# Optimization experiments

Hardware: AMD Instinct MI355X
Metric: run time of the kernel (lower is better)

Reference implementation:

```python
import jax, jax.numpy as jnp
import numpy as np


def setup_inputs() -> dict:
    key = jax.random.key(0)
    ks = jax.random.split(key, 12)
    B, T, E, H, D, NB, BS = 64, 1, 1280, 20, 64, 7, 64
    w = lambda k: jax.random.normal(k, (E, E), jnp.float32) * 0.02
    return {
        "hidden_states": jax.random.normal(ks[0], (B, T, E), jnp.float32),
        "kcache": jax.random.normal(ks[1], (B, H, NB, BS, D), jnp.float32),
        "vcache": jax.random.normal(ks[2], (B, H, NB, BS, D), jnp.float32),
        "wq": w(ks[3]), "bq": jax.random.normal(ks[4], (E,), jnp.float32) * 0.02,
        "wk": w(ks[5]), "bk": jnp.zeros((E,), jnp.float32),
        "wv": w(ks[6]), "bv": jax.random.normal(ks[7], (E,), jnp.float32) * 0.02,
        "wo": w(ks[8]), "bo": jax.random.normal(ks[9], (E,), jnp.float32) * 0.02,
        "cache_position": jax.random.randint(ks[10], (B,), 0, 447, jnp.int32),
        "block_tables": jax.random.randint(ks[11], (B, NB), 0, NB, jnp.int32),
    }


def reference(hidden_states, kcache, vcache, wq, bq, wk, bk, wv, bv, wo, bo,
              cache_position, block_tables):
    B, T, E = hidden_states.shape          # T == 1 (decode)
    _, H, NB, BS, D = kcache.shape
    L = NB * BS                             # max logical cache length (448)
    scaling = D ** -0.5

    # projections -> (B, H, T, D)
    q = (hidden_states @ wq.T + bq).reshape(B, T, H, D).transpose(0, 2, 1, 3) * scaling
    kn = (hidden_states @ wk.T + bk).reshape(B, T, H, D).transpose(0, 2, 1, 3)
    vn = (hidden_states @ wv.T + bv).reshape(B, T, H, D).transpose(0, 2, 1, 3)

    # paged block-table gather: logical cache (B, H, L, D)
    bt = block_tables[:, None, :, None, None].astype(jnp.int32)
    kc = jnp.take_along_axis(kcache, bt, axis=2).reshape(B, H, L, D)
    vc = jnp.take_along_axis(vcache, bt, axis=2).reshape(B, H, L, D)

    # insert the new token's k/v at position cache_position[b]
    pos = jnp.arange(L, dtype=jnp.int32)
    seq = cache_position.reshape(B, 1, 1, 1)
    at_new = pos.reshape(1, 1, L, 1) == seq          # (B,1,L,1)
    k_full = jnp.where(at_new, kn, kc)               # kn (B,H,1,D) broadcasts
    v_full = jnp.where(at_new, vn, vc)

    # causal decode: attend to positions <= cache_position
    scores = jnp.einsum('bhtd,bhld->bhtl', q, k_full)
    valid = pos.reshape(1, 1, 1, L) <= cache_position.reshape(B, 1, 1, 1)
    scores = jnp.where(valid, scores, jnp.finfo(scores.dtype).min)
    probs = jax.nn.softmax(scores, axis=-1)
    out = jnp.einsum('bhtl,bhld->bhtd', probs, v_full)

    out = out.transpose(0, 2, 1, 3).reshape(B, T, E)
    return out @ wo.T + bo
```

## Files before the change

kernel.cpp:

```cpp
#include <hip/hip_runtime.h>
#include <math.h>

#define E 1280
#define NHEAD 20
#define HD 64
#define NBLK 7
#define NBATCH 64

typedef __bf16 bf16x8 __attribute__((ext_vector_type(8)));
typedef float floatx4 __attribute__((ext_vector_type(4)));

__device__ __forceinline__ float wave_max64(float v) {
#pragma unroll
    for (int o = 32; o > 0; o >>= 1) v = fmaxf(v, __shfl_xor(v, o, 64));
    return v;
}
__device__ __forceinline__ float wave_sum64(float v) {
#pragma unroll
    for (int o = 32; o > 0; o >>= 1) v += __shfl_xor(v, o, 64);
    return v;
}
__device__ __forceinline__ bf16x8 cvt8(float4 lo, float4 hi) {
    bf16x8 r;
    r[0] = (__bf16)lo.x; r[1] = (__bf16)lo.y; r[2] = (__bf16)lo.z; r[3] = (__bf16)lo.w;
    r[4] = (__bf16)hi.x; r[5] = (__bf16)hi.y; r[6] = (__bf16)hi.z; r[7] = (__bf16)hi.w;
    return r;
}

template<int NTOT, bool QKV>
__global__ __launch_bounds__(256) void mfma_gemm(
    const float* __restrict__ A,
    const float* __restrict__ W0, const float* __restrict__ W1,
    const float* __restrict__ W2,
    const float* __restrict__ b0, const float* __restrict__ b1,
    const float* __restrict__ b2,
    float* __restrict__ C)
{
    __shared__ __align__(16) float Cred[4][64][16];

    const int t = threadIdx.x;
    const int lane = t & 63;
    const int wv = t >> 6;
    const int quad = lane >> 4;
    const int l16 = lane & 15;
    const int jg0 = blockIdx.x * 16;

    int j0; const float* Wp; const float* bp; float scl;
    if (QKV) {
        const int msel = jg0 / E;
        j0 = jg0 - msel * E;
        Wp = (msel == 0) ? W0 : ((msel == 1) ? W1 : W2);
        bp = (msel == 0) ? b0 : ((msel == 1) ? b1 : b2);
        scl = (msel == 0) ? 0.125f : 1.0f;
    } else { j0 = jg0; Wp = W0; bp = b0; scl = 1.0f; }

    const int kbeg = wv * (E / 4);
    const int ko = quad * 8;

    const float* __restrict__ wrow = Wp + (size_t)(j0 + l16) * E;
    const float* __restrict__ arow = A + (size_t)l16 * E;

    floatx4 acc[4] = {};
    float4 Ac[16], Wc[4];

    {
        const int k0 = kbeg;
#pragma unroll
        for (int rg = 0; rg < 4; ++rg) {
            const float* ar = arow + (size_t)rg * 16 * E + k0 + ko;
            Ac[rg * 4 + 0] = *(const float4*)(ar);
            Ac[rg * 4 + 1] = *(const float4*)(ar + 4);
            Ac[rg * 4 + 2] = *(const float4*)(ar + 32);
            Ac[rg * 4 + 3] = *(const float4*)(ar + 36);
        }
        const float* wr = wrow + k0 + ko;
        Wc[0] = *(const float4*)(wr);
        Wc[1] = *(const float4*)(wr + 4);
        Wc[2] = *(const float4*)(wr + 32);
        Wc[3] = *(const float4*)(wr + 36);
    }

#pragma unroll
    for (int c = 0; c < 5; ++c) {
        float4 An[16], Wn[4];
        if (c < 4) {
            const int k1 = kbeg + (c + 1) * 64;
#pragma unroll
            for (int rg = 0; rg < 4; ++rg) {
                const float* ar = arow + (size_t)rg * 16 * E + k1 + ko;
                An[rg * 4 + 0] = *(const float4*)(ar);
                An[rg * 4 + 1] = *(const float4*)(ar + 4);
                An[rg * 4 + 2] = *(const float4*)(ar + 32);
                An[rg * 4 + 3] = *(const float4*)(ar + 36);
            }
            const float* wr = wrow + k1 + ko;
            Wn[0] = *(const float4*)(wr);
            Wn[1] = *(const float4*)(wr + 4);
            Wn[2] = *(const float4*)(wr + 32);
            Wn[3] = *(const float4*)(wr + 36);
        }
        const bf16x8 bf0 = cvt8(Wc[0], Wc[1]);
        const bf16x8 bf1 = cvt8(Wc[2], Wc[3]);
#pragma unroll
        for (int rg = 0; rg < 4; ++rg) {
            acc[rg] = __builtin_amdgcn_mfma_f32_16x16x32_bf16(
                cvt8(Ac[rg * 4 + 0], Ac[rg * 4 + 1]), bf0, acc[rg], 0, 0, 0);
            acc[rg] = __builtin_amdgcn_mfma_f32_16x16x32_bf16(
                cvt8(Ac[rg * 4 + 2], Ac[rg * 4 + 3]), bf1, acc[rg], 0, 0, 0);
        }
        if (c < 4) {
#pragma unroll
            for (int i = 0; i < 16; ++i) Ac[i] = An[i];
#pragma unroll
            for (int i = 0; i < 4; ++i) Wc[i] = Wn[i];
        }
    }

#pragma unroll
    for (int rg = 0; rg < 4; ++rg)
#pragma unroll
        for (int r = 0; r < 4; ++r)
            Cred[wv][rg * 16 + quad * 4 + r][l16] = acc[rg][r];
    __syncthreads();
#pragma unroll
    for (int i = 0; i < 4; ++i) {
        const int e = t + i * 256;
        const int row = e >> 4, col = e & 15;
        float s = Cred[0][row][col] + Cred[1][row][col]
                + Cred[2][row][col] + Cred[3][row][col];
        C[(size_t)row * NTOT + jg0 + col] = (s + bp[j0 + col]) * scl;
    }
}

__global__ __launch_bounds__(256) void attn_kernel(
    const float* __restrict__ qkv,
    const float* __restrict__ kcache, const float* __restrict__ vcache,
    const int* __restrict__ cache_position, const int* __restrict__ block_tables,
    float* __restrict__ obuf)
{
    const int bh = blockIdx.x;
    const int b = bh / NHEAD;
    const int h = bh - b * NHEAD;
    const int lane = threadIdx.x & 63;
    const int wv = threadIdx.x >> 6;
    const int d4 = lane & 15;
    const int sg = lane >> 4;

    __shared__ __align__(16) float q_lds[64];
    __shared__ __align__(16) float o_lds[4][64];
    __shared__ float ml_lds[4][2];

    const int pos = cache_position[b];
    const int last = pos - 1;
    const int col = h * HD + lane;

    const float qd  = qkv[(size_t)b * (3 * E) + col];
    const float knd = qkv[(size_t)b * (3 * E) + E + col];
    const float vnd = qkv[(size_t)b * (3 * E) + 2 * E + col];
    if (wv == 0) q_lds[lane] = qd;
    __syncthreads();

    float m = -INFINITY, lsum = 0.0f;
    float4 vacc = make_float4(0.f, 0.f, 0.f, 0.f);

    const int nb0 = wv;
    const int nb1 = wv + 4;
    const bool hasb0 = (nb0 * 64 <= last);
    const bool hasb1 = (nb1 * 64 <= last);

    if (hasb0) {
        const size_t bhoff = (size_t)(b * NHEAD + h) * NBLK;
        const int phys0 = block_tables[b * NBLK + nb0];
        const float* __restrict__ Kb0 = kcache + ((bhoff + phys0) << 12);
        const float* __restrict__ Vb0 = vcache + ((bhoff + phys0) << 12);
        const float* __restrict__ Kb1 = Kb0;
        const float* __restrict__ Vb1 = Vb0;
        if (hasb1) {
            const int phys1 = block_tables[b * NBLK + nb1];
            Kb1 = kcache + ((bhoff + phys1) << 12);
            Vb1 = vcache + ((bhoff + phys1) << 12);
        }

        float sc0 = 0.0f, sc1 = -INFINITY;
        {
            const float4* Krow = (const float4*)(Kb0 + lane * HD);
#pragma unroll
            for (int dd = 0; dd < 16; ++dd) {
                float4 k4 = Krow[dd];
                float4 q4 = ((const float4*)q_lds)[dd];
                sc0 = fmaf(k4.x, q4.x, sc0);
                sc0 = fmaf(k4.y, q4.y, sc0);
                sc0 = fmaf(k4.z, q4.z, sc0);
                sc0 = fmaf(k4.w, q4.w, sc0);
            }
            if (nb0 * 64 + lane > last) sc0 = -INFINITY;
        }
        if (hasb1) {
            float s1 = 0.0f;
            const float4* Krow = (const float4*)(Kb1 + lane * HD);
#pragma unroll
            for (int dd = 0; dd < 16; ++dd) {
                float4 k4 = Krow[dd];
                float4 q4 = ((const float4*)q_lds)[dd];
                s1 = fmaf(k4.x, q4.x, s1);
                s1 = fmaf(k4.y, q4.y, s1);
                s1 = fmaf(k4.z, q4.z, s1);
                s1 = fmaf(k4.w, q4.w, s1);
            }
            sc1 = (nb1 * 64 + lane > last) ? -INFINITY : s1;
        }

        float4 v0r[16];
#pragma unroll
        for (int j = 0; j < 16; ++j)
            v0r[j] = *(const float4*)&Vb0[(sg + 4 * j) * HD + d4 * 4];

        const float m_ = wave_max64(fmaxf(sc0, sc1));
        const float p0 = __expf(sc0 - m_);
        const float p1 = __expf(sc1 - m_);
        lsum = wave_sum64(p0 + p1);
        m = m_;

#pragma unroll
        for (int j = 0; j < 16; ++j) {
            const float ps = __shfl(p0, sg + 4 * j, 64);
            vacc.x = fmaf(ps, v0r[j].x, vacc.x);
            vacc.y = fmaf(ps, v0r[j].y, vacc.y);
            vacc.z = fmaf(ps, v0r[j].z, vacc.z);
            vacc.w = fmaf(ps, v0r[j].w, vacc.w);
        }
        if (hasb1) {
#pragma unroll
            for (int j = 0; j < 16; ++j) {
                const int s = sg + 4 * j;
                const float ps = __shfl(p1, s, 64);
                float4 v4 = *(const float4*)&Vb1[s * HD + d4 * 4];
                vacc.x = fmaf(ps, v4.x, vacc.x);
                vacc.y = fmaf(ps, v4.y, vacc.y);
                vacc.z = fmaf(ps, v4.z, vacc.z);
                vacc.w = fmaf(ps, v4.w, vacc.w);
            }
        }
    }

#pragma unroll
    for (int o = 16; o <= 32; o <<= 1) {
        vacc.x += __shfl_xor(vacc.x, o, 64);
        vacc.y += __shfl_xor(vacc.y, o, 64);
        vacc.z += __shfl_xor(vacc.z, o, 64);
        vacc.w += __shfl_xor(vacc.w, o, 64);
    }
    if (sg == 0) *(float4*)&o_lds[wv][d4 * 4] = vacc;
    if (lane == 0) { ml_lds[wv][0] = m; ml_lds[wv][1] = lsum; }
    __syncthreads();

    if (wv == 0) {
        const float qk = wave_sum64(qd * knd);
        float Mf = qk;
#pragma unroll
        for (int w = 0; w < 4; ++w) Mf = fmaxf(Mf, ml_lds[w][0]);
        float osum = 0.0f, Ls = 0.0f;
#pragma unroll
        for (int w = 0; w < 4; ++w) {
            const float f = __expf(ml_lds[w][0] - Mf);
            osum = fmaf(o_lds[w][lane], f, osum);
            Ls   = fmaf(ml_lds[w][1], f, Ls);
        }
        const float pn = __expf(qk - Mf);
        osum = fmaf(pn, vnd, osum);
        Ls += pn;
        obuf[(size_t)b * E + h * HD + lane] = osum / Ls;
    }
}

extern "C" void kernel_launch(void* const* d_in, const int* in_sizes, int n_in,
                              void* d_out, int out_size, void* d_ws, size_t ws_size,
                              hipStream_t stream) {
    const float* hidden = (const float*)d_in[0];
    const float* kcache = (const float*)d_in[1];
    const float* vcache = (const float*)d_in[2];
    const float* wq = (const float*)d_in[3];
    const float* bq = (const float*)d_in[4];
    const float* wk = (const float*)d_in[5];
    const float* bk = (const float*)d_in[6];
    const float* wvp = (const float*)d_in[7];
    const float* bv = (const float*)d_in[8];
    const float* wo = (const float*)d_in[9];
    const float* bo = (const float*)d_in[10];
    const int* cpos = (const int*)d_in[11];
    const int* btab = (const int*)d_in[12];
    float* out = (float*)d_out;

    float* ws = (float*)d_ws;
    float* qkv = ws;
    float* ob  = ws + 64 * 3 * E;

    mfma_gemm<3 * E, true><<<(3 * E) / 16, 256, 0, stream>>>(
        hidden, wq, wk, wvp, bq, bk, bv, qkv);
    attn_kernel<<<NBATCH * NHEAD, 256, 0, stream>>>(qkv, kcache, vcache, cpos, btab, ob);
    mfma_gemm<E, false><<<E / 16, 256, 0, stream>>>(
        ob, wo, wo, wo, bo, bo, bo, out);
}
```

Before: 326.3 us.

## Fuse attention and output projection into one launch with atomic grid sync

Merges the attention kernel and the output-projection GEMM into a single launch. The extra GEMM blocks prefetch their first slice of wo, then spin on a global flag that the last attention block sets through an atomic counter; the counter is reset inside the QKV GEMM kernel. This removes one kernel launch boundary and lets the wo prefetch overlap attention. It risks deadlock if the spinning blocks are scheduled before attention blocks can finish, and the spinning blocks occupy CU slots. The QK dot product also now uses two partial accumulators to shorten its dependency chain.

New measurement: 682.3 us. +109.1%, slower.

```diff
diff --git a/kernel.cpp b/kernel.cpp
--- a/kernel.cpp
+++ b/kernel.cpp
@@ -6,6 +6,8 @@
 #define HD 64
 #define NBLK 7
 #define NBATCH 64
+#define NUNIT (NBATCH * NHEAD)
+#define NTILE_O (E / 16)
 
 typedef __bf16 bf16x8 __attribute__((ext_vector_type(8)));
 typedef float floatx4 __attribute__((ext_vector_type(4)));
@@ -27,16 +29,17 @@
     return r;
 }
 
-template<int NTOT, bool QKV>
-__global__ __launch_bounds__(256) void mfma_gemm(
+__global__ __launch_bounds__(256) void qkv_gemm(
     const float* __restrict__ A,
     const float* __restrict__ W0, const float* __restrict__ W1,
     const float* __restrict__ W2,
     const float* __restrict__ b0, const float* __restrict__ b1,
     const float* __restrict__ b2,
-    float* __restrict__ C)
+    float* __restrict__ C, int* __restrict__ sync)
 {
     __shared__ __align__(16) float Cred[4][64][16];
+
+    if (blockIdx.x == 0 && threadIdx.x == 0) { sync[0] = 0; sync[1] = 0; }
 
     const int t = threadIdx.x;
     const int lane = t & 63;
@@ -45,14 +48,11 @@
     const int l16 = lane & 15;
     const int jg0 = blockIdx.x * 16;
 
-    int j0; const float* Wp; const float* bp; float scl;
-    if (QKV) {
-        const int msel = jg0 / E;
-        j0 = jg0 - msel * E;
-        Wp = (msel == 0) ? W0 : ((msel == 1) ? W1 : W2);
-        bp = (msel == 0) ? b0 : ((msel == 1) ? b1 : b2);
-        scl = (msel == 0) ? 0.125f : 1.0f;
-    } else { j0 = jg0; Wp = W0; bp = b0; scl = 1.0f; }
+    const int msel = jg0 / E;
+    const int j0 = jg0 - msel * E;
+    const float* Wp = (msel == 0) ? W0 : ((msel == 1) ? W1 : W2);
+    const float* bp = (msel == 0) ? b0 : ((msel == 1) ? b1 : b2);
+    const float scl = (msel == 0) ? 0.125f : 1.0f;
 
     const int kbeg = wv * (E / 4);
     const int ko = quad * 8;
@@ -128,148 +128,236 @@
         const int row = e >> 4, col = e & 15;
         float s = Cred[0][row][col] + Cred[1][row][col]
                 + Cred[2][row][col] + Cred[3][row][col];
-        C[(size_t)row * NTOT + jg0 + col] = (s + bp[j0 + col]) * scl;
-    }
-}
-
-__global__ __launch_bounds__(256) void attn_kernel(
+        C[(size_t)row * (3 * E) + jg0 + col] = (s + bp[j0 + col]) * scl;
+    }
+}
+
+__global__ __launch_bounds__(256, 4) void attn_oproj(
     const float* __restrict__ qkv,
     const float* __restrict__ kcache, const float* __restrict__ vcache,
     const int* __restrict__ cache_position, const int* __restrict__ block_tables,
-    float* __restrict__ obuf)
+    float* __restrict__ ob,
+    const float* __restrict__ wo, const float* __restrict__ bo,
+    float* __restrict__ out, int* __restrict__ sync)
 {
-    const int bh = blockIdx.x;
-    const int b = bh / NHEAD;
-    const int h = bh - b * NHEAD;
-    const int lane = threadIdx.x & 63;
-    const int wv = threadIdx.x >> 6;
-    const int d4 = lane & 15;
-    const int sg = lane >> 4;
-
-    __shared__ __align__(16) float q_lds[64];
-    __shared__ __align__(16) float o_lds[4][64];
-    __shared__ float ml_lds[4][2];
-
-    const int pos = cache_position[b];
-    const int last = pos - 1;
-    const int col = h * HD + lane;
-
-    const float qd  = qkv[(size_t)b * (3 * E) + col];
-    const float knd = qkv[(size_t)b * (3 * E) + E + col];
-    const float vnd = qkv[(size_t)b * (3 * E) + 2 * E + col];
-    if (wv == 0) q_lds[lane] = qd;
+    __shared__ __align__(16) float smem[4096];
+
+    const int t = threadIdx.x;
+    const int lane = t & 63;
+    const int wv = t >> 6;
+
+    if (blockIdx.x < NUNIT) {
+        float* q_lds = smem;
+        float (*o_lds)[64] = (float (*)[64])(smem + 64);
+        float* ml_lds = smem + 64 + 256;
+
+        const int bh = blockIdx.x;
+        const int b = bh / NHEAD;
+        const int h = bh - b * NHEAD;
+        const int d4 = lane & 15;
+        const int sg = lane >> 4;
+
+        const int pos = cache_position[b];
+        const int last = pos - 1;
+        const int col = h * HD + lane;
+
+        const float qd  = qkv[(size_t)b * (3 * E) + col];
+        const float knd = qkv[(size_t)b * (3 * E) + E + col];
+        const float vnd = qkv[(size_t)b * (3 * E) + 2 * E + col];
+        if (wv == 0) q_lds[lane] = qd;
+        __syncthreads();
+
+        float m = -INFINITY, lsum = 0.0f;
+        float4 vacc = make_float4(0.f, 0.f, 0.f, 0.f);
+
+        const int nb0 = wv;
+        const int nb1 = wv + 4;
+        const bool hasb0 = (nb0 * 64 <= last);
+        const bool hasb1 = (nb1 * 64 <= last);
+
+        if (hasb0) {
+            const size_t bhoff = (size_t)(b * NHEAD + h) * NBLK;
+            const int phys0 = block_tables[b * NBLK + nb0];
+            const float* __restrict__ Kb0 = kcache + ((bhoff + phys0) << 12);
+            const float* __restrict__ Vb0 = vcache + ((bhoff + phys0) << 12);
+            const float* __restrict__ Kb1 = Kb0;
+            const float* __restrict__ Vb1 = Vb0;
+            if (hasb1) {
+                const int phys1 = block_tables[b * NBLK + nb1];
+                Kb1 = kcache + ((bhoff + phys1) << 12);
+                Vb1 = vcache + ((bhoff + phys1) << 12);
+            }
+
+            float sc0 = 0.0f, sc1 = -INFINITY;
+            {
+                const float4* Krow = (const float4*)(Kb0 + lane * HD);
+                float sa = 0.f, sb = 0.f;
+#pragma unroll
+                for (int dd = 0; dd < 16; dd += 2) {
+                    float4 k4 = Krow[dd],     q4 = ((const float4*)q_lds)[dd];
+                    float4 k5 = Krow[dd + 1], q5 = ((const float4*)q_lds)[dd + 1];
+                    sa = fmaf(k4.x, q4.x, sa); sa = fmaf(k4.y, q4.y, sa);
+                    sa = fmaf(k4.z, q4.z, sa); sa = fmaf(k4.w, q4.w, sa);
+                    sb = fmaf(k5.x, q5.x, sb); sb = fmaf(k5.y, q5.y, sb);
+                    sb = fmaf(k5.z, q5.z, sb); sb = fmaf(k5.w, q5.w, sb);
+                }
+                sc0 = sa + sb;
+                if (nb0 * 64 + lane > last) sc0 = -INFINITY;
+            }
+            if (hasb1) {
+                const float4* Krow = (const float4*)(Kb1 + lane * HD);
+                float sa = 0.f, sb = 0.f;
+#pragma unroll
+                for (int dd = 0; dd < 16; dd += 2) {
+                    float4 k4 = Krow[dd],     q4 = ((const float4*)q_lds)[dd];
+                    float4 k5 = Krow[dd + 1], q5 = ((const float4*)q_lds)[dd + 1];
+                    sa = fmaf(k4.x, q4.x, sa); sa = fmaf(k4.y, q4.y, sa);
+                    sa = fmaf(k4.z, q4.z, sa); sa = fmaf(k4.w, q4.w, sa);
+                    sb = fmaf(k5.x, q5.x, sb); sb = fmaf(k5.y, q5.y, sb);
+                    sb = fmaf(k5.z, q5.z, sb); sb = fmaf(k5.w, q5.w, sb);
+                }
+                sc1 = (nb1 * 64 + lane > last) ? -INFINITY : (sa + sb);
+            }
+
+            float4 v0r[16];
+#pragma unroll
+            for (int j = 0; j < 16; ++j)
+                v0r[j] = *(const float4*)&Vb0[(sg + 4 * j) * HD + d4 * 4];
+
+            const float m_ = wave_max64(fmaxf(sc0, sc1));
+            const float p0 = __expf(sc0 - m_);
+            const float p1 = __expf(sc1 - m_);
+            lsum = wave_sum64(p0 + p1);
+            m = m_;
+
+#pragma unroll
+            for (int j = 0; j < 16; ++j) {
+                const float ps = __shfl(p0, sg + 4 * j, 64);
+                vacc.x = fmaf(ps, v0r[j].x, vacc.x);
+                vacc.y = fmaf(ps, v0r[j].y, vacc.y);
+                vacc.z = fmaf(ps, v0r[j].z, vacc.z);
+                vacc.w = fmaf(ps, v0r[j].w, vacc.w);
+            }
+            if (hasb1) {
+#pragma unroll
+                for (int j = 0; j < 16; ++j) {
+                    const int s = sg + 4 * j;
+                    const float ps = __shfl(p1, s, 64);
+                    float4 v4 = *(const float4*)&Vb1[s * HD + d4 * 4];
+                    vacc.x = fmaf(ps, v4.x, vacc.x);
+                    vacc.y = fmaf(ps, v4.y, vacc.y);
+                    vacc.z = fmaf(ps, v4.z, vacc.z);
+                    vacc.w = fmaf(ps, v4.w, vacc.w);
+                }
+            }
+        }
+
+#pragma unroll
+        for (int o = 16; o <= 32; o <<= 1) {
+            vacc.x += __shfl_xor(vacc.x, o, 64);
+            vacc.y += __shfl_xor(vacc.y, o, 64);
+            vacc.z += __shfl_xor(vacc.z, o, 64);
+            vacc.w += __shfl_xor(vacc.w, o, 64);
+        }
+        if (sg == 0) *(float4*)&o_lds[wv][d4 * 4] = vacc;
+        if (lane == 0) { ml_lds[wv * 2 + 0] = m; ml_lds[wv * 2 + 1] = lsum; }
+        __syncthreads();
+
+        if (wv == 0) {
+            const float qk = wave_sum64(qd * knd);
+            float Mf = qk;
+#pragma unroll
+            for (int w = 0; w < 4; ++w) Mf = fmaxf(Mf, ml_lds[w * 2]);
+            float osum = 0.0f, Ls = 0.0f;
+#pragma unroll
+            for (int w = 0; w < 4; ++w) {
+                const float f = __expf(ml_lds[w * 2] - Mf);
+                osum = fmaf(o_lds[w][lane], f, osum);
+                Ls   = fmaf(ml_lds[w * 2 + 1], f, Ls);
+            }
+            const float pn = __expf(qk - Mf);
+            osum = fmaf(pn, vnd, osum);
+            Ls += pn;
+            ob[(size_t)b * E + h * HD + lane] = osum / Ls;
+        }
+
+        __threadfence();
+        __syncthreads();
+        if (t == 0) {
+            if (__hip_atomic_fetch_add(&sync[0], 1, __ATOMIC_ACQ_REL,
+                                       __HIP_MEMORY_SCOPE_AGENT) == NUNIT - 1)
+                __hip_atomic_store(&sync[1], 1, __ATOMIC_RELEASE,
+                                   __HIP_MEMORY_SCOPE_AGENT);
+        }
+        return;
+    }
+
+    const int jg0 = (blockIdx.x - NUNIT) * 16;
+    const int quad = lane >> 4;
+    const int l16 = lane & 15;
+    const int kbeg = wv * (E / 4);
+    const int ko = quad * 8;
+    const float* __restrict__ wrow = wo + (size_t)(jg0 + l16) * E;
+
+    float4 Wc[4];
+    {
+        const float* wr = wrow + kbeg + ko;
+        Wc[0] = *(const float4*)(wr);
+        Wc[1] = *(const float4*)(wr + 4);
+        Wc[2] = *(const float4*)(wr + 32);
+        Wc[3] = *(const float4*)(wr + 36);
+    }
+
+    while (__hip_atomic_load(&sync[1], __ATOMIC_ACQUIRE,
+                             __HIP_MEMORY_SCOPE_AGENT) == 0)
+        __builtin_amdgcn_s_sleep(8);
+
+    floatx4 acc[4] = {};
+#pragma unroll
+    for (int c = 0; c < 5; ++c) {
+        float4 Wn[4];
+        if (c < 4) {
+            const float* wr = wrow + kbeg + (c + 1) * 64 + ko;
+            Wn[0] = *(const float4*)(wr);
+            Wn[1] = *(const float4*)(wr + 4);
+            Wn[2] = *(const float4*)(wr + 32);
+            Wn[3] = *(const float4*)(wr + 36);
+        }
+        const bf16x8 bf0 = cvt8(Wc[0], Wc[1]);
+        const bf16x8 bf1 = cvt8(Wc[2], Wc[3]);
+        const int k0 = kbeg + c * 64 + ko;
+#pragma unroll
+        for (int rg = 0; rg < 4; ++rg) {
+            const float* ar = ob + (size_t)(rg * 16 + l16) * E + k0;
+            float4 a0 = *(const float4*)(ar);
+            float4 a1 = *(const float4*)(ar + 4);
+            float4 a2 = *(const float4*)(ar + 32);
+            float4 a3 = *(const float4*)(ar + 36);
+            acc[rg] = __builtin_amdgcn_mfma_f32_16x16x32_bf16(
+                cvt8(a0, a1), bf0, acc[rg], 0, 0, 0);
+            acc[rg] = __builtin_amdgcn_mfma_f32_16x16x32_bf16(
+                cvt8(a2, a3), bf1, acc[rg], 0, 0, 0);
+        }
+        if (c < 4) {
+#pragma unroll
+            for (int i = 0; i < 4; ++i) Wc[i] = Wn[i];
+        }
+    }
+
+    float (*Cred)[64][16] = (float (*)[64][16])smem;
+#pragma unroll
+    for (int rg = 0; rg < 4; ++rg)
+#pragma unroll
+        for (int r = 0; r < 4; ++r)
+            Cred[wv][rg * 16 + quad * 4 + r][l16] = acc[rg][r];
     __syncthreads();
-
-    float m = -INFINITY, lsum = 0.0f;
-    float4 vacc = make_float4(0.f, 0.f, 0.f, 0.f);
-
-    const int nb0 = wv;
-    const int nb1 = wv + 4;
-    const bool hasb0 = (nb0 * 64 <= last);
-    const bool hasb1 = (nb1 * 64 <= last);
-
-    if (hasb0) {
-        const size_t bhoff = (size_t)(b * NHEAD + h) * NBLK;
-        const int phys0 = block_tables[b * NBLK + nb0];
-        const float* __restrict__ Kb0 = kcache + ((bhoff + phys0) << 12);
-        const float* __restrict__ Vb0 = vcache + ((bhoff + phys0) << 12);
-        const float* __restrict__ Kb1 = Kb0;
-        const float* __restrict__ Vb1 = Vb0;
-        if (hasb1) {
-            const int phys1 = block_tables[b * NBLK + nb1];
-            Kb1 = kcache + ((bhoff + phys1) << 12);
-            Vb1 = vcache + ((bhoff + phys1) << 12);
-        }
-
-        float sc0 = 0.0f, sc1 = -INFINITY;
-        {
-            const float4* Krow = (const float4*)(Kb0 + lane * HD);
-#pragma unroll
-            for (int dd = 0; dd < 16; ++dd) {
-                float4 k4 = Krow[dd];
-                float4 q4 = ((const float4*)q_lds)[dd];
-                sc0 = fmaf(k4.x, q4.x, sc0);
-                sc0 = fmaf(k4.y, q4.y, sc0);
-                sc0 = fmaf(k4.z, q4.z, sc0);
-                sc0 = fmaf(k4.w, q4.w, sc0);
-            }
-            if (nb0 * 64 + lane > last) sc0 = -INFINITY;
-        }
-        if (hasb1) {
-            float s1 = 0.0f;
-            const float4* Krow = (const float4*)(Kb1 + lane * HD);
-#pragma unroll
-            for (int dd = 0; dd < 16; ++dd) {
-                float4 k4 = Krow[dd];
-                float4 q4 = ((const float4*)q_lds)[dd];
-                s1 = fmaf(k4.x, q4.x, s1);
-                s1 = fmaf(k4.y, q4.y, s1);
-                s1 = fmaf(k4.z, q4.z, s1);
-                s1 = fmaf(k4.w, q4.w, s1);
-            }
-            sc1 = (nb1 * 64 + lane > last) ? -INFINITY : s1;
-        }
-
-        float4 v0r[16];
-#pragma unroll
-        for (int j = 0; j < 16; ++j)
-            v0r[j] = *(const float4*)&Vb0[(sg + 4 * j) * HD + d4 * 4];
-
-        const float m_ = wave_max64(fmaxf(sc0, sc1));
-        const float p0 = __expf(sc0 - m_);
-        const float p1 = __expf(sc1 - m_);
-        lsum = wave_sum64(p0 + p1);
-        m = m_;
-
-#pragma unroll
-        for (int j = 0; j < 16; ++j) {
-            const float ps = __shfl(p0, sg + 4 * j, 64);
-            vacc.x = fmaf(ps, v0r[j].x, vacc.x);
-            vacc.y = fmaf(ps, v0r[j].y, vacc.y);
-            vacc.z = fmaf(ps, v0r[j].z, vacc.z);
-            vacc.w = fmaf(ps, v0r[j].w, vacc.w);
-        }
-        if (hasb1) {
-#pragma unroll
-            for (int j = 0; j < 16; ++j) {
-                const int s = sg + 4 * j;
-                const float ps = __shfl(p1, s, 64);
-                float4 v4 = *(const float4*)&Vb1[s * HD + d4 * 4];
-                vacc.x = fmaf(ps, v4.x, vacc.x);
-                vacc.y = fmaf(ps, v4.y, vacc.y);
-                vacc.z = fmaf(ps, v4.z, vacc.z);
-                vacc.w = fmaf(ps, v4.w, vacc.w);
-            }
-        }
-    }
-
-#pragma unroll
-    for (int o = 16; o <= 32; o <<= 1) {
-        vacc.x += __shfl_xor(vacc.x, o, 64);
-        vacc.y += __shfl_xor(vacc.y, o, 64);
-        vacc.z += __shfl_xor(vacc.z, o, 64);
-        vacc.w += __shfl_xor(vacc.w, o, 64);
-    }
-    if (sg == 0) *(float4*)&o_lds[wv][d4 * 4] = vacc;
-    if (lane == 0) { ml_lds[wv][0] = m; ml_lds[wv][1] = lsum; }
-    __syncthreads();
-
-    if (wv == 0) {
-        const float qk = wave_sum64(qd * knd);
-        float Mf = qk;
-#pragma unroll
-        for (int w = 0; w < 4; ++w) Mf = fmaxf(Mf, ml_lds[w][0]);
-        float osum = 0.0f, Ls = 0.0f;
-#pragma unroll
-        for (int w = 0; w < 4; ++w) {
-            const float f = __expf(ml_lds[w][0] - Mf);
-            osum = fmaf(o_lds[w][lane], f, osum);
-            Ls   = fmaf(ml_lds[w][1], f, Ls);
-        }
-        const float pn = __expf(qk - Mf);
-        osum = fmaf(pn, vnd, osum);
-        Ls += pn;
-        obuf[(size_t)b * E + h * HD + lane] = osum / Ls;
+#pragma unroll
+    for (int i = 0; i < 4; ++i) {
+        const int e = t + i * 256;
+        const int row = e >> 4, ccol = e & 15;
+        float s = Cred[0][row][ccol] + Cred[1][row][ccol]
+                + Cred[2][row][ccol] + Cred[3][row][ccol];
+        out[(size_t)row * E + jg0 + ccol] = s + bo[jg0 + ccol];
     }
 }
 
@@ -294,10 +382,10 @@
     float* ws = (float*)d_ws;
     float* qkv = ws;
     float* ob  = ws + 64 * 3 * E;
-
-    mfma_gemm<3 * E, true><<<(3 * E) / 16, 256, 0, stream>>>(
-        hidden, wq, wk, wvp, bq, bk, bv, qkv);
-    attn_kernel<<<NBATCH * NHEAD, 256, 0, stream>>>(qkv, kcache, vcache, cpos, btab, ob);
-    mfma_gemm<E, false><<<E / 16, 256, 0, stream>>>(
-        ob, wo, wo, wo, bo, bo, bo, out);
-}
+    int* sync  = (int*)(ws + 64 * 3 * E + 64 * E);
+
+    qkv_gemm<<<(3 * E) / 16, 256, 0, stream>>>(
+        hidden, wq, wk, wvp, bq, bk, bv, qkv, sync);
+    attn_oproj<<<NUNIT + NTILE_O, 256, 0, stream>>>(
+        qkv, kcache, vcache, cpos, btab, ob, wo, bo, out, sync);
+}
```

## Fuse output projection into attention kernel via atomics, skip masked K/V loads

Applied to the files above, without the earlier changes.

The separate output-projection GEMM launch is removed. Each (batch, head) attention block now multiplies its 64-wide head output against the matching slice of wo and atomically adds into the output, which the QKV GEMM pre-initialises with the bias. K/V loads are also predicated so positions past the causal limit are not fetched, and the dot products use two accumulators. The cost is 1280 blocks each reading a 1280x64 strip of wo with strided float4 loads, about 20x redundant wo traffic across batches, plus heavy atomic contention on the output, replacing one MFMA GEMM.

Result: slower. 377.3 us (+15.6%).

```diff
diff --git a/kernel.cpp b/kernel.cpp
--- a/kernel.cpp
+++ b/kernel.cpp
@@ -6,6 +6,7 @@
 #define HD 64
 #define NBLK 7
 #define NBATCH 64
+#define NUNIT (NBATCH * NHEAD)
 
 typedef __bf16 bf16x8 __attribute__((ext_vector_type(8)));
 typedef float floatx4 __attribute__((ext_vector_type(4)));
@@ -27,32 +28,36 @@
     return r;
 }
 
-template<int NTOT, bool QKV>
-__global__ __launch_bounds__(256) void mfma_gemm(
+__global__ __launch_bounds__(256) void qkv_gemm(
     const float* __restrict__ A,
     const float* __restrict__ W0, const float* __restrict__ W1,
     const float* __restrict__ W2,
     const float* __restrict__ b0, const float* __restrict__ b1,
     const float* __restrict__ b2,
-    float* __restrict__ C)
+    float* __restrict__ C,
+    const float* __restrict__ bo, float* __restrict__ out)
 {
     __shared__ __align__(16) float Cred[4][64][16];
 
     const int t = threadIdx.x;
+
+    if (blockIdx.x < 80) {
+        const int flat4 = blockIdx.x * 256 + t;
+        const int j4 = flat4 % (E / 4);
+        ((float4*)out)[flat4] = ((const float4*)bo)[j4];
+    }
+
     const int lane = t & 63;
     const int wv = t >> 6;
     const int quad = lane >> 4;
     const int l16 = lane & 15;
     const int jg0 = blockIdx.x * 16;
 
-    int j0; const float* Wp; const float* bp; float scl;
-    if (QKV) {
-        const int msel = jg0 / E;
-        j0 = jg0 - msel * E;
-        Wp = (msel == 0) ? W0 : ((msel == 1) ? W1 : W2);
-        bp = (msel == 0) ? b0 : ((msel == 1) ? b1 : b2);
-        scl = (msel == 0) ? 0.125f : 1.0f;
-    } else { j0 = jg0; Wp = W0; bp = b0; scl = 1.0f; }
+    const int msel = jg0 / E;
+    const int j0 = jg0 - msel * E;
+    const float* Wp = (msel == 0) ? W0 : ((msel == 1) ? W1 : W2);
+    const float* bp = (msel == 0) ? b0 : ((msel == 1) ? b1 : b2);
+    const float scl = (msel == 0) ? 0.125f : 1.0f;
 
     const int kbeg = wv * (E / 4);
     const int ko = quad * 8;
@@ -128,27 +133,30 @@
         const int row = e >> 4, col = e & 15;
         float s = Cred[0][row][col] + Cred[1][row][col]
                 + Cred[2][row][col] + Cred[3][row][col];
-        C[(size_t)row * NTOT + jg0 + col] = (s + bp[j0 + col]) * scl;
-    }
-}
-
-__global__ __launch_bounds__(256) void attn_kernel(
+        C[(size_t)row * (3 * E) + jg0 + col] = (s + bp[j0 + col]) * scl;
+    }
+}
+
+__global__ __launch_bounds__(256) void attn_oproj(
     const float* __restrict__ qkv,
     const float* __restrict__ kcache, const float* __restrict__ vcache,
     const int* __restrict__ cache_position, const int* __restrict__ block_tables,
-    float* __restrict__ obuf)
+    const float* __restrict__ wo,
+    float* __restrict__ out)
 {
+    __shared__ __align__(16) float q_lds[64];
+    __shared__ __align__(16) float o_lds[4][64];
+    __shared__ __align__(16) float o_final[64];
+    __shared__ float ml_lds[8];
+
     const int bh = blockIdx.x;
     const int b = bh / NHEAD;
     const int h = bh - b * NHEAD;
-    const int lane = threadIdx.x & 63;
-    const int wv = threadIdx.x >> 6;
+    const int t = threadIdx.x;
+    const int lane = t & 63;
+    const int wv = t >> 6;
     const int d4 = lane & 15;
     const int sg = lane >> 4;
-
-    __shared__ __align__(16) float q_lds[64];
-    __shared__ __align__(16) float o_lds[4][64];
-    __shared__ float ml_lds[4][2];
 
     const int pos = cache_position[b];
     const int last = pos - 1;
@@ -169,6 +177,8 @@
     const bool hasb1 = (nb1 * 64 <= last);
 
     if (hasb0) {
+        const int ll0 = last - nb0 * 64;
+        const int ll1 = last - nb1 * 64;
         const size_t bhoff = (size_t)(b * NHEAD + h) * NBLK;
         const int phys0 = block_tables[b * NBLK + nb0];
         const float* __restrict__ Kb0 = kcache + ((bhoff + phys0) << 12);
@@ -181,39 +191,45 @@
             Vb1 = vcache + ((bhoff + phys1) << 12);
         }
 
-        float sc0 = 0.0f, sc1 = -INFINITY;
-        {
+        float sc0 = -INFINITY, sc1 = -INFINITY;
+        if (lane <= ll0) {
             const float4* Krow = (const float4*)(Kb0 + lane * HD);
-#pragma unroll
-            for (int dd = 0; dd < 16; ++dd) {
-                float4 k4 = Krow[dd];
-                float4 q4 = ((const float4*)q_lds)[dd];
-                sc0 = fmaf(k4.x, q4.x, sc0);
-                sc0 = fmaf(k4.y, q4.y, sc0);
-                sc0 = fmaf(k4.z, q4.z, sc0);
-                sc0 = fmaf(k4.w, q4.w, sc0);
+            float sa = 0.f, sb = 0.f;
+#pragma unroll
+            for (int dd = 0; dd < 16; dd += 2) {
+                float4 k4 = Krow[dd],     q4 = ((const float4*)q_lds)[dd];
+                float4 k5 = Krow[dd + 1], q5 = ((const float4*)q_lds)[dd + 1];
+                sa = fmaf(k4.x, q4.x, sa); sa = fmaf(k4.y, q4.y, sa);
+                sa = fmaf(k4.z, q4.z, sa); sa = fmaf(k4.w, q4.w, sa);
+                sb = fmaf(k5.x, q5.x, sb); sb = fmaf(k5.y, q5.y, sb);
+                sb = fmaf(k5.z, q5.z, sb); sb = fmaf(k5.w, q5.w, sb);
             }
-            if (nb0 * 64 + lane > last) sc0 = -INFINITY;
-        }
-        if (hasb1) {
-            float s1 = 0.0f;
+            sc0 = sa + sb;
+        }
+        if (hasb1 && lane <= ll1) {
             const float4* Krow = (const float4*)(Kb1 + lane * HD);
-#pragma unroll
-            for (int dd = 0; dd < 16; ++dd) {
-                float4 k4 = Krow[dd];
-                float4 q4 = ((const float4*)q_lds)[dd];
-                s1 = fmaf(k4.x, q4.x, s1);
-                s1 = fmaf(k4.y, q4.y, s1);
-                s1 = fmaf(k4.z, q4.z, s1);
-                s1 = fmaf(k4.w, q4.w, s1);
+            float sa = 0.f, sb = 0.f;
+#pragma unroll
+            for (int dd = 0; dd < 16; dd += 2) {
+                float4 k4 = Krow[dd],     q4 = ((const float4*)q_lds)[dd];
+                float4 k5 = Krow[dd + 1], q5 = ((const float4*)q_lds)[dd + 1];
+                sa = fmaf(k4.x, q4.x, sa); sa = fmaf(k4.y, q4.y, sa);
+                sa = fmaf(k4.z, q4.z, sa); sa = fmaf(k4.w, q4.w, sa);
+                sb = fmaf(k5.x, q5.x, sb); sb = fmaf(k5.y, q5.y, sb);
+                sb = fmaf(k5.z, q5.z, sb); sb = fmaf(k5.w, q5.w, sb);
             }
-            sc1 = (nb1 * 64 + lane > last) ? -INFINITY : s1;
+            sc1 = sa + sb;
         }
 
         float4 v0r[16];
 #pragma unroll
-        for (int j = 0; j < 16; ++j)
-            v0r[j] = *(const float4*)&Vb0[(sg + 4 * j) * HD + d4 * 4];
+        for (int j = 0; j < 16; ++j) {
+            const int s = sg + 4 * j;
+            if (s <= ll0)
+                v0r[j] = *(const float4*)&Vb0[s * HD + d4 * 4];
+            else
+                v0r[j] = make_float4(0.f, 0.f, 0.f, 0.f);
+        }
 
         const float m_ = wave_max64(fmaxf(sc0, sc1));
         const float p0 = __expf(sc0 - m_);
@@ -234,11 +250,13 @@
             for (int j = 0; j < 16; ++j) {
                 const int s = sg + 4 * j;
                 const float ps = __shfl(p1, s, 64);
-                float4 v4 = *(const float4*)&Vb1[s * HD + d4 * 4];
-                vacc.x = fmaf(ps, v4.x, vacc.x);
-                vacc.y = fmaf(ps, v4.y, vacc.y);
-                vacc.z = fmaf(ps, v4.z, vacc.z);
-                vacc.w = fmaf(ps, v4.w, vacc.w);
+                if (s <= ll1) {
+                    float4 v4 = *(const float4*)&Vb1[s * HD + d4 * 4];
+                    vacc.x = fmaf(ps, v4.x, vacc.x);
+                    vacc.y = fmaf(ps, v4.y, vacc.y);
+                    vacc.z = fmaf(ps, v4.z, vacc.z);
+                    vacc.w = fmaf(ps, v4.w, vacc.w);
+                }
             }
         }
     }
@@ -251,25 +269,44 @@
         vacc.w += __shfl_xor(vacc.w, o, 64);
     }
     if (sg == 0) *(float4*)&o_lds[wv][d4 * 4] = vacc;
-    if (lane == 0) { ml_lds[wv][0] = m; ml_lds[wv][1] = lsum; }
+    if (lane == 0) { ml_lds[wv * 2 + 0] = m; ml_lds[wv * 2 + 1] = lsum; }
     __syncthreads();
 
     if (wv == 0) {
         const float qk = wave_sum64(qd * knd);
         float Mf = qk;
 #pragma unroll
-        for (int w = 0; w < 4; ++w) Mf = fmaxf(Mf, ml_lds[w][0]);
+        for (int w = 0; w < 4; ++w) Mf = fmaxf(Mf, ml_lds[w * 2]);
         float osum = 0.0f, Ls = 0.0f;
 #pragma unroll
         for (int w = 0; w < 4; ++w) {
-            const float f = __expf(ml_lds[w][0] - Mf);
+            const float f = __expf(ml_lds[w * 2] - Mf);
             osum = fmaf(o_lds[w][lane], f, osum);
-            Ls   = fmaf(ml_lds[w][1], f, Ls);
+            Ls   = fmaf(ml_lds[w * 2 + 1], f, Ls);
         }
         const float pn = __expf(qk - Mf);
         osum = fmaf(pn, vnd, osum);
         Ls += pn;
-        obuf[(size_t)b * E + h * HD + lane] = osum / Ls;
+        o_final[lane] = osum / Ls;
+    }
+    __syncthreads();
+
+    const float4* of4 = (const float4*)o_final;
+#pragma unroll
+    for (int i = 0; i < 5; ++i) {
+        const int j = t + i * 256;
+        const float4* wr = (const float4*)(wo + (size_t)j * E + h * HD);
+        float sa = 0.f, sb = 0.f;
+#pragma unroll
+        for (int dd = 0; dd < 16; dd += 2) {
+            float4 w4 = wr[dd],     o4 = of4[dd];
+            float4 w5 = wr[dd + 1], o5 = of4[dd + 1];
+            sa = fmaf(w4.x, o4.x, sa); sa = fmaf(w4.y, o4.y, sa);
+            sa = fmaf(w4.z, o4.z, sa); sa = fmaf(w4.w, o4.w, sa);
+            sb = fmaf(w5.x, o5.x, sb); sb = fmaf(w5.y, o5.y, sb);
+            sb = fmaf(w5.z, o5.z, sb); sb = fmaf(w5.w, o5.w, sb);
+        }
+        atomicAdd(&out[(size_t)b * E + j], sa + sb);
     }
 }
 
@@ -291,13 +328,10 @@
     const int* btab = (const int*)d_in[12];
     float* out = (float*)d_out;
 
-    float* ws = (float*)d_ws;
-    float* qkv = ws;
-    float* ob  = ws + 64 * 3 * E;
-
-    mfma_gemm<3 * E, true><<<(3 * E) / 16, 256, 0, stream>>>(
-        hidden, wq, wk, wvp, bq, bk, bv, qkv);
-    attn_kernel<<<NBATCH * NHEAD, 256, 0, stream>>>(qkv, kcache, vcache, cpos, btab, ob);
-    mfma_gemm<E, false><<<E / 16, 256, 0, stream>>>(
-        ob, wo, wo, wo, bo, bo, bo, out);
-}
+    float* qkv = (float*)d_ws;
+
+    qkv_gemm<<<(3 * E) / 16, 256, 0, stream>>>(
+        hidden, wq, wk, wvp, bq, bk, bv, qkv, bo, out);
+    attn_oproj<<<NUNIT, 256, 0, stream>>>(
+        qkv, kcache, vcache, cpos, btab, wo, out);
+}
```
